# Optimization experiments

Measured on AMD Instinct MI355X. Metric: run time of the kernel, lower is better.

The kernel has to match this reference:

```python
import jax, jax.numpy as jnp
import numpy as np

N = 10000
E = 160000
IN_CH = 128
HID = 128
HEADS = 4
OUT_CH = 1  # forced by nn.Linear(heads, 1) applied after conv2


def _linear_params(key, out_f, in_f):
    k1, k2 = jax.random.split(key)
    bound = 1.0 / np.sqrt(in_f)
    W = jax.random.uniform(k1, (out_f, in_f), jnp.float32, -bound, bound)
    b = jax.random.uniform(k2, (out_f,), jnp.float32, -bound, bound)
    return W, b


def setup_inputs() -> dict:
    key = jax.random.key(0)
    ks = jax.random.split(key, 12)
    x = jax.random.normal(ks[0], (N, IN_CH), jnp.float32)
    edge_index = jax.random.randint(ks[1], (2, E), 0, N, jnp.int64)

    # conv1: TransformerConv(IN_CH, HID, HEADS)
    Wq1, bq1 = _linear_params(ks[2], HEADS * HID, IN_CH)
    Wk1, bk1 = _linear_params(ks[3], HEADS * HID, IN_CH)
    Wv1, bv1 = _linear_params(ks[4], HEADS * HID, IN_CH)
    Ws1, bs1 = _linear_params(ks[5], HEADS * HID, IN_CH)  # root/skip

    # conv2: TransformerConv(HID*HEADS, OUT_CH, HEADS)
    d2 = HID * HEADS
    Wq2, bq2 = _linear_params(ks[6], HEADS * OUT_CH, d2)
    Wk2, bk2 = _linear_params(ks[7], HEADS * OUT_CH, d2)
    Wv2, bv2 = _linear_params(ks[8], HEADS * OUT_CH, d2)
    Ws2, bs2 = _linear_params(ks[9], HEADS * OUT_CH, d2)

    # final nn.Linear(HEADS, 1)
    Wl, bl = _linear_params(ks[10], 1, HEADS)

    return dict(x=x, edge_index=edge_index,
                Wq1=Wq1, bq1=bq1, Wk1=Wk1, bk1=bk1, Wv1=Wv1, bv1=bv1, Ws1=Ws1, bs1=bs1,
                Wq2=Wq2, bq2=bq2, Wk2=Wk2, bk2=bk2, Wv2=Wv2, bv2=bv2, Ws2=Ws2, bs2=bs2,
                Wl=Wl, bl=bl)


def transformer_conv(x, edge_index, Wq, bq, Wk, bk, Wv, bv, Ws, bs, heads, ch):
    # PyG TransformerConv defaults: concat=True, root_weight=True, beta=False
    n = x.shape[0]
    q = (x @ Wq.T + bq).reshape(n, heads, ch)
    k = (x @ Wk.T + bk).reshape(n, heads, ch)
    v = (x @ Wv.T + bv).reshape(n, heads, ch)

    src, dst = edge_index[0], edge_index[1]  # messages flow src -> dst
    # per-edge attention logits [E, H]
    logits = jnp.einsum('ehc,ehc->eh', q[dst], k[src]) / np.sqrt(ch).astype(np.float32)

    # segment softmax over edges grouped by destination node
    seg_max = jax.ops.segment_max(logits, dst, num_segments=n)  # [N, H]
    seg_max = jnp.where(jnp.isfinite(seg_max), seg_max, 0.0)
    ex = jnp.exp(logits - seg_max[dst])
    denom = jax.ops.segment_sum(ex, dst, num_segments=n)  # [N, H]
    alpha = ex / jnp.maximum(denom[dst], 1e-16)  # [E, H]

    # scatter-aggregate weighted values
    msgs = alpha[:, :, None] * v[src]  # [E, H, C]
    out = jax.ops.segment_sum(msgs, dst, num_segments=n)  # [N, H, C]
    out = out.reshape(n, heads * ch)
    # root/skip connection
    return out + (x @ Ws.T + bs)


def reference(x, edge_index,
              Wq1, bq1, Wk1, bk1, Wv1, bv1, Ws1, bs1,
              Wq2, bq2, Wk2, bk2, Wv2, bv2, Ws2, bs2,
              Wl, bl):
    h = transformer_conv(x, edge_index, Wq1, bq1, Wk1, bk1, Wv1, bv1, Ws1, bs1, HEADS, HID)
    h = jax.nn.relu(h)
    # dropout is identity in eval mode
    h = transformer_conv(h, edge_index, Wq2, bq2, Wk2, bk2, Wv2, bv2, Ws2, bs2, HEADS, OUT_CH)
    h = h @ Wl.T + bl  # [N, 1]
    return jnp.mean(h, axis=0, keepdims=True)  # [1, 1]
```

## Files before the change

kernel.cpp:

```cpp
#include <hip/hip_runtime.h>
#include <math.h>

#define NN 10000
#define NE 160000
#define NROWT 79
#define NGEMM (NROWT * 32)

typedef __attribute__((ext_vector_type(8))) short bf16x8;
typedef __attribute__((ext_vector_type(4))) float f32x4;
typedef __attribute__((ext_vector_type(2))) float f32x2;

#if defined(__has_builtin)
#if __has_builtin(__builtin_amdgcn_cvt_pk_fp8_f32) && __has_builtin(__builtin_amdgcn_cvt_pk_f32_fp8)
#define HW_FP8 1
#endif
#endif

__device__ inline ushort f2bf(float x) {
  uint u = __float_as_uint(x);
  return (ushort)((u + 0x7fffu + ((u >> 16) & 1u)) >> 16);
}
__device__ inline uint pk2bf(float a, float b) {
  return (uint)f2bf(a) | ((uint)f2bf(b) << 16);
}

__device__ inline void unpack8(uint4 u, float* f) {
  f[0] = __uint_as_float(u.x << 16); f[1] = __uint_as_float(u.x & 0xffff0000u);
  f[2] = __uint_as_float(u.y << 16); f[3] = __uint_as_float(u.y & 0xffff0000u);
  f[4] = __uint_as_float(u.z << 16); f[5] = __uint_as_float(u.z & 0xffff0000u);
  f[6] = __uint_as_float(u.w << 16); f[7] = __uint_as_float(u.w & 0xffff0000u);
}

#ifndef HW_FP8
__device__ inline float fp8_dec1(uint b) {
  uint s = b >> 7, e = (b >> 3) & 15, m = b & 7;
  float v = (e == 0) ? ldexpf((float)m, -9) : ldexpf((float)(8 + m), (int)e - 10);
  return s ? -v : v;
}
__device__ inline uint fp8_enc1(float x) {
  uint s = (__float_as_uint(x) >> 31) << 7;
  float a = fabsf(x);
  if (!(a < 448.f)) return s | 0x7e;
  if (a < 9.765625e-4f) return s;
  int e; float m = frexpf(a, &e);
  int E = e - 1, q;
  if (E < -6) {
    q = (int)rintf(ldexpf(a, 9));
    if (q == 0) return s;
    if (q >= 8) return s | 8;
    return s | (uint)q;
  }
  q = (int)rintf(ldexpf(m, 4));
  if (q == 16) { q = 8; ++E; }
  if (E > 8 || (E == 8 && q == 15)) return s | 0x7e;
  return s | ((uint)(E + 7) << 3) | (uint)(q - 8);
}
#endif

__device__ inline uint pack4_fp8(float a, float b, float c, float d) {
#ifdef HW_FP8
  uint w = (uint)__builtin_amdgcn_cvt_pk_fp8_f32(a, b, 0, false);
  w = (uint)__builtin_amdgcn_cvt_pk_fp8_f32(c, d, (int)w, true);
  return w;
#else
  return fp8_enc1(a) | (fp8_enc1(b) << 8) | (fp8_enc1(c) << 16) | (fp8_enc1(d) << 24);
#endif
}

__device__ inline void dec8_fp8(uint lo, uint hi, float* f) {
#ifdef HW_FP8
  f32x2 p0 = __builtin_amdgcn_cvt_pk_f32_fp8((int)lo, false);
  f32x2 p1 = __builtin_amdgcn_cvt_pk_f32_fp8((int)lo, true);
  f32x2 p2 = __builtin_amdgcn_cvt_pk_f32_fp8((int)hi, false);
  f32x2 p3 = __builtin_amdgcn_cvt_pk_f32_fp8((int)hi, true);
  f[0] = p0.x; f[1] = p0.y; f[2] = p1.x; f[3] = p1.y;
  f[4] = p2.x; f[5] = p2.y; f[6] = p3.x; f[7] = p3.y;
#else
  f[0] = fp8_dec1(lo & 255); f[1] = fp8_dec1((lo >> 8) & 255);
  f[2] = fp8_dec1((lo >> 16) & 255); f[3] = fp8_dec1(lo >> 24);
  f[4] = fp8_dec1(hi & 255); f[5] = fp8_dec1((hi >> 8) & 255);
  f[6] = fp8_dec1((hi >> 16) & 255); f[7] = fp8_dec1(hi >> 24);
#endif
}

__device__ inline void dec16(uint4 u, float* f) {
  dec8_fp8(u.x, u.y, f);
  dec8_fp8(u.z, u.w, f + 8);
}

__global__ __launch_bounds__(1024) void zero_k(
    int* __restrict__ deg, float* __restrict__ out)
{
  int i = blockIdx.x * 1024 + threadIdx.x;
  if (i < NN) deg[i] = 0;
  if (i == 0) out[0] = 0.f;
}

__global__ __launch_bounds__(256) void prep_k(
    const float* __restrict__ x,
    const float* __restrict__ Wq1, const float* __restrict__ Wk1,
    const float* __restrict__ Wv1, const float* __restrict__ Ws1,
    ushort* __restrict__ x_bf, ushort* __restrict__ w1bf,
    const int* __restrict__ dst, int* __restrict__ deg)
{
  int i = blockIdx.x * 256 + threadIdx.x;
  if (i < NE) atomicAdd(&deg[dst[i]], 1);
  const int n4x = NN * 32;
  const int n4w = 512 * 128 / 4;
  if (i < n4x) {
    float4 v = ((const float4*)x)[i];
    ushort4 o;
    o.x = f2bf(v.x); o.y = f2bf(v.y); o.z = f2bf(v.z); o.w = f2bf(v.w);
    ((ushort4*)x_bf)[i] = o;
  } else {
    int c = i - n4x;
    if (c < 4 * n4w) {
      int seg = c >> 14, k = c & 16383;
      const float* W = (seg == 0) ? Wq1 : (seg == 1) ? Wk1
                     : (seg == 2) ? Wv1 : Ws1;
      float4 v = ((const float4*)W)[k];
      ushort4 o;
      o.x = f2bf(v.x); o.y = f2bf(v.y); o.z = f2bf(v.z); o.w = f2bf(v.w);
      ((ushort4*)(w1bf + ((size_t)seg << 16)))[k] = o;
    }
  }
}

__global__ __launch_bounds__(1024) void scan_k(
    const int* __restrict__ deg, int* __restrict__ rowptr,
    int* __restrict__ cursor)
{
  __shared__ int wsum[16];
  int tid = threadIdx.x;
  int base = tid * 10;
  int loc[10]; int s = 0;
  #pragma unroll
  for (int i = 0; i < 10; ++i) {
    int v = (base + i < NN) ? deg[base + i] : 0;
    loc[i] = s; s += v;
  }
  int mysum = s;
  #pragma unroll
  for (int d = 1; d < 64; d <<= 1) {
    int v = __shfl_up(s, d);
    if ((tid & 63) >= d) s += v;
  }
  if ((tid & 63) == 63) wsum[tid >> 6] = s;
  __syncthreads();
  int woff = 0;
  for (int w = 0; w < (tid >> 6); ++w) woff += wsum[w];
  int excl = woff + s - mysum;
  #pragma unroll
  for (int i = 0; i < 10; ++i) {
    int idx = base + i;
    if (idx < NN) { int r = excl + loc[i]; rowptr[idx] = r; cursor[idx] = r; }
  }
  if (tid == 1023) rowptr[NN] = woff + s;
}

__global__ __launch_bounds__(256) void gemm_scatter(
    const ushort* __restrict__ xbf, const ushort* __restrict__ wbf,
    const float* __restrict__ bq, const float* __restrict__ bk,
    const float* __restrict__ bv, const float* __restrict__ bs,
    unsigned char* __restrict__ q8, unsigned char* __restrict__ kv8,
    ushort* __restrict__ h1b,
    const int* __restrict__ src, const int* __restrict__ dst,
    int* __restrict__ cursor, int* __restrict__ csr_src)
{
  if (blockIdx.x >= NGEMM) {
    int e = (blockIdx.x - NGEMM) * 256 + threadIdx.x;
    if (e < NE) {
      int pos = atomicAdd(&cursor[dst[e]], 1);
      csr_src[pos] = src[e];
    }
    return;
  }
  __shared__ __align__(16) ushort LDSbuf[24576];
  ushort* Al = LDSbuf;
  ushort* Bl = LDSbuf + 16384;
  const int row0 = (blockIdx.x % NROWT) << 7;
  const int ncol0 = (blockIdx.x / NROWT) << 6;
  const int tid = threadIdx.x;

  #pragma unroll
  for (int i = 0; i < 8; ++i) {
    int slot = tid + (i << 8);
    int r = slot >> 4, c = slot & 15;
    int gr = row0 + r;
    uint4 v = make_uint4(0u, 0u, 0u, 0u);
    if (gr < NN) v = *(const uint4*)(xbf + (size_t)gr * 128 + (c << 3));
    *(uint4*)(Al + r * 128 + ((c ^ (r & 7)) << 3)) = v;
  }
  #pragma unroll
  for (int i = 0; i < 4; ++i) {
    int slot = tid + (i << 8);
    int r = slot >> 4, c = slot & 15;
    uint4 v = *(const uint4*)(wbf + (size_t)(ncol0 + r) * 128 + (c << 3));
    *(uint4*)(Bl + r * 128 + ((c ^ (r & 7)) << 3)) = v;
  }
  __syncthreads();

  const int wid = tid >> 6, lane = tid & 63;
  const int wm = wid >> 1, wn = wid & 1;
  const int lr = lane & 15, lkg = lane >> 4;
  const int seg = ncol0 >> 9;
  const int colInSeg = ncol0 & 511;
  const bool swp = (seg < 3);

  f32x4 acc[4][2];
  #pragma unroll
  for (int m = 0; m < 4; ++m)
    #pragma unroll
    for (int n = 0; n < 2; ++n) acc[m][n] = (f32x4){0.f, 0.f, 0.f, 0.f};

  #pragma unroll
  for (int ks = 0; ks < 4; ++ks) {
    int c16 = (ks << 2) + lkg;
    bf16x8 a[4], b[2];
    #pragma unroll
    for (int mf = 0; mf < 4; ++mf) {
      int r = (wm << 6) + (mf << 4) + lr;
      a[mf] = *(const bf16x8*)(Al + r * 128 + ((c16 ^ (r & 7)) << 3));
    }
    #pragma unroll
    for (int nf = 0; nf < 2; ++nf) {
      int r = (wn << 5) + (nf << 4) + lr;
      b[nf] = *(const bf16x8*)(Bl + r * 128 + ((c16 ^ (r & 7)) << 3));
    }
    if (swp) {
      #pragma unroll
      for (int mf = 0; mf < 4; ++mf)
        #pragma unroll
        for (int nf = 0; nf < 2; ++nf)
          acc[mf][nf] = __builtin_amdgcn_mfma_f32_16x16x32_bf16(
              b[nf], a[mf], acc[mf][nf], 0, 0, 0);
    } else {
      #pragma unroll
      for (int mf = 0; mf < 4; ++mf)
        #pragma unroll
        for (int nf = 0; nf < 2; ++nf)
          acc[mf][nf] = __builtin_amdgcn_mfma_f32_16x16x32_bf16(
              a[mf], b[nf], acc[mf][nf], 0, 0, 0);
    }
  }

  __syncthreads();
  float* S = (float*)LDSbuf;
  const float* bias = (seg == 0) ? bq : (seg == 1) ? bk : (seg == 2) ? bv : bs;

  if (swp) {
    const float scale = (seg == 0) ? 0.08838834764831845f : 1.f;
    #pragma unroll
    for (int mf = 0; mf < 4; ++mf) {
      int rl = (wm << 6) + (mf << 4) + lr;
      #pragma unroll
      for (int nf = 0; nf < 2; ++nf) {
        int cl = (wn << 5) + (nf << 4) + (lkg << 2);
        float4 bb = *(const float4*)(bias + colInSeg + cl);
        float4 o;
        o.x = (acc[mf][nf][0] + bb.x) * scale;
        o.y = (acc[mf][nf][1] + bb.y) * scale;
        o.z = (acc[mf][nf][2] + bb.z) * scale;
        o.w = (acc[mf][nf][3] + bb.w) * scale;
        *(float4*)(S + rl * 68 + cl) = o;
      }
    }
    __syncthreads();
    unsigned char* out8 = (seg == 0) ? q8 : kv8;
    const int rs = (seg == 0) ? 512 : 1024;
    const int choff = ((seg == 2) ? 512 : 0) + colInSeg;
    for (int tt = tid; tt < 512; tt += 256) {
      int row = tt >> 2, q4 = (tt & 3) << 4;
      int grow = row0 + row;
      if (grow < NN) {
        const float* p = S + row * 68 + q4;
        uint4 w;
        w.x = pack4_fp8(p[0],  p[1],  p[2],  p[3]);
        w.y = pack4_fp8(p[4],  p[5],  p[6],  p[7]);
        w.z = pack4_fp8(p[8],  p[9],  p[10], p[11]);
        w.w = pack4_fp8(p[12], p[13], p[14], p[15]);
        *(uint4*)(out8 + (size_t)grow * rs + choff + q4) = w;
      }
    }
  } else {
    #pragma unroll
    for (int mf = 0; mf < 4; ++mf) {
      #pragma unroll
      for (int nf = 0; nf < 2; ++nf) {
        int cl = (wn << 5) + (nf << 4) + lr;
        float bb = bias[colInSeg + cl];
        #pragma unroll
        for (int r = 0; r < 4; ++r) {
          int rl = (wm << 6) + (mf << 4) + (lkg << 2) + r;
          S[rl * 68 + cl] = acc[mf][nf][r] + bb;
        }
      }
    }
    __syncthreads();
    {
      int tt = tid;
      int row = tt >> 1, hf = (tt & 1) << 5;
      int grow = row0 + row;
      if (grow < NN) {
        const float* p = S + row * 68 + hf;
        #pragma unroll
        for (int g = 0; g < 4; ++g) {
          uint4 w;
          w.x = pk2bf(p[g*8+0], p[g*8+1]);
          w.y = pk2bf(p[g*8+2], p[g*8+3]);
          w.z = pk2bf(p[g*8+4], p[g*8+5]);
          w.w = pk2bf(p[g*8+6], p[g*8+7]);
          *(uint4*)(h1b + (size_t)grow * 512 + colInSeg + hf + g * 8) = w;
        }
      }
    }
  }
}

#define EDGE_A(kvreg)                                                      \
  {                                                                        \
    float f[16]; dec16(kvreg, f);                                          \
    float t = qf[0]*f[0]+qf[1]*f[1]+qf[2]*f[2]+qf[3]*f[3]                  \
            + qf[4]*f[4]+qf[5]*f[5]+qf[6]*f[6]+qf[7]*f[7]                  \
            + qf[8]*f[8]+qf[9]*f[9]+qf[10]*f[10]+qf[11]*f[11]              \
            + qf[12]*f[12]+qf[13]*f[13]+qf[14]*f[14]+qf[15]*f[15];         \
    t += __shfl_xor(t, 1);                                                 \
    t += __shfl_xor(t, 2);                                                 \
    t += __shfl_xor(t, 4);                                                 \
    float exA = __expf(t);                                                 \
    float exO = __shfl_xor(exA, 32);                                       \
    if (kl) den += exA;                                                    \
    float exV = kl ? 0.f : exO;                                            \
    _Pragma("unroll")                                                      \
    for (int i = 0; i < 16; ++i) acc[i] = fmaf(exV, f[i], acc[i]);         \
  }

__global__ __launch_bounds__(256) void attn1(
    const unsigned char* __restrict__ q8, const unsigned char* __restrict__ kv8,
    const int* __restrict__ rowptr, const int* __restrict__ csr_src,
    ushort* __restrict__ h1b)
{
  const int n = blockIdx.x * 4 + (threadIdx.x >> 6);
  const int lane = threadIdx.x & 63;
  const bool kl = lane < 32;
  const int vl = lane & 31;

  float qf[16];
  if (kl) {
    uint4 qv = *(const uint4*)(q8 + (size_t)n * 512 + (lane << 4));
    dec16(qv, qf);
  } else {
    #pragma unroll
    for (int i = 0; i < 16; ++i) qf[i] = 0.f;
  }

  float acc[16] = {};
  float den = 0.f;
  int j = rowptr[n];
  const int e1 = rowptr[n + 1];
  for (; j + 3 < e1; j += 4) {
    int s0 = csr_src[j], s1 = csr_src[j + 1];
    int s2 = csr_src[j + 2], s3 = csr_src[j + 3];
    uint4 a0 = *(const uint4*)(kv8 + (size_t)s0 * 1024 + (lane << 4));
    uint4 a1 = *(const uint4*)(kv8 + (size_t)s1 * 1024 + (lane << 4));
    uint4 a2 = *(const uint4*)(kv8 + (size_t)s2 * 1024 + (lane << 4));
    uint4 a3 = *(const uint4*)(kv8 + (size_t)s3 * 1024 + (lane << 4));
    EDGE_A(a0)
    EDGE_A(a1)
    EDGE_A(a2)
    EDGE_A(a3)
  }
  for (; j < e1; ++j) {
    int s0 = csr_src[j];
    uint4 a0 = *(const uint4*)(kv8 + (size_t)s0 * 1024 + (lane << 4));
    EDGE_A(a0)
  }

  float dAll = kl ? den : 0.f;
  float dv = __shfl_xor(dAll, 32);
  if (!kl) {
    float inv = 1.f / fmaxf(dv, 1e-16f);
    int c0 = vl << 4;
    float sk[16];
    uint4 s0 = *(const uint4*)(h1b + (size_t)n * 512 + c0);
    uint4 s1 = *(const uint4*)(h1b + (size_t)n * 512 + c0 + 8);
    unpack8(s0, sk); unpack8(s1, sk + 8);
    ushort o[16];
    #pragma unroll
    for (int i = 0; i < 16; ++i)
      o[i] = f2bf(fmaxf(sk[i] + acc[i] * inv, 0.f));
    uint4 w0, w1;
    w0.x = (uint)o[0]  | ((uint)o[1]  << 16);
    w0.y = (uint)o[2]  | ((uint)o[3]  << 16);
    w0.z = (uint)o[4]  | ((uint)o[5]  << 16);
    w0.w = (uint)o[6]  | ((uint)o[7]  << 16);
    w1.x = (uint)o[8]  | ((uint)o[9]  << 16);
    w1.y = (uint)o[10] | ((uint)o[11] << 16);
    w1.z = (uint)o[12] | ((uint)o[13] << 16);
    w1.w = (uint)o[14] | ((uint)o[15] << 16);
    *(uint4*)(h1b + (size_t)n * 512 + c0) = w0;
    *(uint4*)(h1b + (size_t)n * 512 + c0 + 8) = w1;
  }
}

__global__ __launch_bounds__(256) void gemm_l2(
    const ushort* __restrict__ h1b,
    const float* __restrict__ Wq, const float* __restrict__ bq,
    const float* __restrict__ Wk, const float* __restrict__ bk,
    const float* __restrict__ Wv, const float* __restrict__ bv,
    const float* __restrict__ Ws, const float* __restrict__ bs,
    float* __restrict__ qkv2, float* __restrict__ acc2)
{
  __shared__ float red[4][64][17];
  int n0 = blockIdx.x * 64;
  int wid = threadIdx.x >> 6, lane = threadIdx.x & 63;
  int n = n0 + lane;
  const float* Wm[4] = {Wq, Wk, Wv, Ws};
  float s[16] = {};
  if (n < NN) {
    const ushort* a = h1b + (size_t)n * 512 + wid * 128;
    #pragma unroll 2
    for (int i = 0; i < 128; i += 8) {
      uint4 hv = *(const uint4*)(a + i);
      float av[8]; unpack8(hv, av);
      #pragma unroll
      for (int j = 0; j < 16; ++j) {
        const float* w = Wm[j >> 2] + (size_t)(j & 3) * 512 + wid * 128 + i;
        s[j] += av[0]*w[0] + av[1]*w[1] + av[2]*w[2] + av[3]*w[3]
              + av[4]*w[4] + av[5]*w[5] + av[6]*w[6] + av[7]*w[7];
      }
    }
  }
  #pragma unroll
  for (int j = 0; j < 16; ++j) red[wid][lane][j] = s[j];
  __syncthreads();
  #pragma unroll
  for (int q = 0; q < 4; ++q) {
    int idx = threadIdx.x * 4 + q;
    int ln = idx >> 4, j = idx & 15;
    int nn2 = n0 + ln;
    if (nn2 >= NN) continue;
    float v = red[0][ln][j] + red[1][ln][j] + red[2][ln][j] + red[3][ln][j];
    int sg = j >> 2, r = j & 3;
    const float* bb = (sg == 0) ? bq : (sg == 1) ? bk : (sg == 2) ? bv : bs;
    v += bb[r];
    if (sg < 3) qkv2[nn2 * 12 + sg * 4 + r] = v;
    else        acc2[nn2 * 4 + r] = v;
  }
}

__global__ __launch_bounds__(256) void attn2_final(
    const float* __restrict__ qkv2, const int* __restrict__ rowptr,
    const int* __restrict__ csr_src, const float* __restrict__ acc2,
    const float* __restrict__ Wl, const float* __restrict__ bl,
    float* __restrict__ out)
{
  __shared__ float red[4];
  int t = blockIdx.x * 256 + threadIdx.x;
  int n = t >> 4, h = (t >> 2) & 3, part = t & 3;
  float q = qkv2[n * 12 + h];
  float den = 0.f, acc = 0.f;
  int e1 = rowptr[n + 1];
  for (int j = rowptr[n] + part; j < e1; j += 4) {
    int s = csr_src[j];
    float k = qkv2[s * 12 + 4 + h];
    float v = qkv2[s * 12 + 8 + h];
    float ex = __expf(q * k);
    den += ex; acc += ex * v;
  }
  den += __shfl_xor(den, 1); acc += __shfl_xor(acc, 1);
  den += __shfl_xor(den, 2); acc += __shfl_xor(acc, 2);
  float c = 0.f;
  if (part == 0)
    c = (acc2[n * 4 + h] + acc / fmaxf(den, 1e-16f)) * Wl[h] * (1.0f / NN);
  if (t == 0) c += bl[0];
  c += __shfl_xor(c, 4);
  c += __shfl_xor(c, 8);
  c += __shfl_xor(c, 16);
  c += __shfl_xor(c, 32);
  if ((threadIdx.x & 63) == 0) red[threadIdx.x >> 6] = c;
  __syncthreads();
  if (threadIdx.x == 0)
    unsafeAtomicAdd(out, red[0] + red[1] + red[2] + red[3]);
}

extern "C" void kernel_launch(void* const* d_in, const int* in_sizes, int n_in,
                              void* d_out, int out_size, void* d_ws, size_t ws_size,
                              hipStream_t stream)
{
  const float* x   = (const float*)d_in[0];
  const int*   ei  = (const int*)d_in[1];
  const float *Wq1 = (const float*)d_in[2],  *bq1 = (const float*)d_in[3];
  const float *Wk1 = (const float*)d_in[4],  *bk1 = (const float*)d_in[5];
  const float *Wv1 = (const float*)d_in[6],  *bv1 = (const float*)d_in[7];
  const float *Ws1 = (const float*)d_in[8],  *bs1 = (const float*)d_in[9];
  const float *Wq2 = (const float*)d_in[10], *bq2 = (const float*)d_in[11];
  const float *Wk2 = (const float*)d_in[12], *bk2 = (const float*)d_in[13];
  const float *Wv2 = (const float*)d_in[14], *bv2 = (const float*)d_in[15];
  const float *Ws2 = (const float*)d_in[16], *bs2 = (const float*)d_in[17];
  const float *Wl  = (const float*)d_in[18], *bl  = (const float*)d_in[19];
  const int* srcp = ei;
  const int* dstp = ei + NE;

  unsigned char* q8  = (unsigned char*)d_ws;
  unsigned char* kv8 = q8 + (size_t)NN * 512;
  ushort* x_bf = (ushort*)(kv8 + (size_t)NN * 1024);
  ushort* w1bf = x_bf + (size_t)NN * 128;
  ushort* h1b  = w1bf + (size_t)2048 * 128;
  float*  qkv2 = (float*)(h1b + (size_t)NN * 512);
  float*  acc2 = qkv2 + (size_t)NN * 12;
  int*   deg     = (int*)(acc2 + (size_t)NN * 4);
  int*   rowptr  = deg + NN;
  int*   cursor  = rowptr + NN + 1;
  int*   csr_src = cursor + NN;

  zero_k<<<10, 1024, 0, stream>>>(deg, (float*)d_out);
  {
    const int total = NN * 32 + 4 * (512 * 128 / 4);
    prep_k<<<(total + 255) / 256, 256, 0, stream>>>(
        x, Wq1, Wk1, Wv1, Ws1, x_bf, w1bf, dstp, deg);
  }
  scan_k<<<1, 1024, 0, stream>>>(deg, rowptr, cursor);

  gemm_scatter<<<NGEMM + (NE + 255) / 256, 256, 0, stream>>>(
      x_bf, w1bf, bq1, bk1, bv1, bs1, q8, kv8, h1b,
      srcp, dstp, cursor, csr_src);

  attn1<<<NN / 4, 256, 0, stream>>>(q8, kv8, rowptr, csr_src, h1b);

  gemm_l2<<<(NN + 63) / 64, 256, 0, stream>>>(
      h1b, Wq2, bq2, Wk2, bk2, Wv2, bv2, Ws2, bs2, qkv2, acc2);

  attn2_final<<<NN * 16 / 256, 256, 0, stream>>>(
      qkv2, rowptr, csr_src, acc2, Wl, bl, (float*)d_out);
}
```

Before: 131.6 us.

## Widen GEMM column tile to 128 and unroll edge gather loop by eight

The GEMM tile grows from 128x64 to 128x128 output columns, halving the number of GEMM blocks. Each wave now computes 32 rows by 128 columns, so every A fragment is reused across more B fragments, and the epilogue drains through LDS in two passes. The attention edge loop is unrolled to eight outstanding KV gathers per iteration to expose more memory-level parallelism. In exchange the kernel uses more LDS and more accumulator registers, which may lower occupancy, and the two-pass epilogue adds extra barriers.

After: 131.2 us, median of 3. About the same (-0.3%).

```diff
diff --git a/kernel.cpp b/kernel.cpp
--- a/kernel.cpp
+++ b/kernel.cpp
@@ -4,7 +4,8 @@
 #define NN 10000
 #define NE 160000
 #define NROWT 79
-#define NGEMM (NROWT * 32)
+#define NCOLT 16
+#define NGEMM (NROWT * NCOLT)
 
 typedef __attribute__((ext_vector_type(8))) short bf16x8;
 typedef __attribute__((ext_vector_type(4))) float f32x4;
@@ -175,11 +176,11 @@
     }
     return;
   }
-  __shared__ __align__(16) ushort LDSbuf[24576];
+  __shared__ __align__(16) ushort LDSbuf[32768];
   ushort* Al = LDSbuf;
   ushort* Bl = LDSbuf + 16384;
   const int row0 = (blockIdx.x % NROWT) << 7;
-  const int ncol0 = (blockIdx.x / NROWT) << 6;
+  const int ncol0 = (blockIdx.x / NROWT) << 7;
   const int tid = threadIdx.x;
 
   #pragma unroll
@@ -192,7 +193,7 @@
     *(uint4*)(Al + r * 128 + ((c ^ (r & 7)) << 3)) = v;
   }
   #pragma unroll
-  for (int i = 0; i < 4; ++i) {
+  for (int i = 0; i < 8; ++i) {
     int slot = tid + (i << 8);
     int r = slot >> 4, c = slot & 15;
     uint4 v = *(const uint4*)(wbf + (size_t)(ncol0 + r) * 128 + (c << 3));
@@ -200,45 +201,44 @@
   }
   __syncthreads();
 
-  const int wid = tid >> 6, lane = tid & 63;
-  const int wm = wid >> 1, wn = wid & 1;
+  const int wv = tid >> 6, lane = tid & 63;
   const int lr = lane & 15, lkg = lane >> 4;
   const int seg = ncol0 >> 9;
   const int colInSeg = ncol0 & 511;
   const bool swp = (seg < 3);
 
-  f32x4 acc[4][2];
-  #pragma unroll
-  for (int m = 0; m < 4; ++m)
-    #pragma unroll
-    for (int n = 0; n < 2; ++n) acc[m][n] = (f32x4){0.f, 0.f, 0.f, 0.f};
+  f32x4 acc[2][8];
+  #pragma unroll
+  for (int m = 0; m < 2; ++m)
+    #pragma unroll
+    for (int n = 0; n < 8; ++n) acc[m][n] = (f32x4){0.f, 0.f, 0.f, 0.f};
 
   #pragma unroll
   for (int ks = 0; ks < 4; ++ks) {
     int c16 = (ks << 2) + lkg;
-    bf16x8 a[4], b[2];
-    #pragma unroll
-    for (int mf = 0; mf < 4; ++mf) {
-      int r = (wm << 6) + (mf << 4) + lr;
+    bf16x8 a[2], b[8];
+    #pragma unroll
+    for (int mf = 0; mf < 2; ++mf) {
+      int r = (wv << 5) + (mf << 4) + lr;
       a[mf] = *(const bf16x8*)(Al + r * 128 + ((c16 ^ (r & 7)) << 3));
     }
     #pragma unroll
-    for (int nf = 0; nf < 2; ++nf) {
-      int r = (wn << 5) + (nf << 4) + lr;
+    for (int nf = 0; nf < 8; ++nf) {
+      int r = (nf << 4) + lr;
       b[nf] = *(const bf16x8*)(Bl + r * 128 + ((c16 ^ (r & 7)) << 3));
     }
     if (swp) {
       #pragma unroll
-      for (int mf = 0; mf < 4; ++mf)
+      for (int mf = 0; mf < 2; ++mf)
         #pragma unroll
-        for (int nf = 0; nf < 2; ++nf)
+        for (int nf = 0; nf < 8; ++nf)
           acc[mf][nf] = __builtin_amdgcn_mfma_f32_16x16x32_bf16(
               b[nf], a[mf], acc[mf][nf], 0, 0, 0);
     } else {
       #pragma unroll
-      for (int mf = 0; mf < 4; ++mf)
+      for (int mf = 0; mf < 2; ++mf)
         #pragma unroll
-        for (int nf = 0; nf < 2; ++nf)
+        for (int nf = 0; nf < 8; ++nf)
           acc[mf][nf] = __builtin_amdgcn_mfma_f32_16x16x32_bf16(
               a[mf], b[nf], acc[mf][nf], 0, 0, 0);
     }
@@ -250,69 +250,75 @@
 
   if (swp) {
     const float scale = (seg == 0) ? 0.08838834764831845f : 1.f;
-    #pragma unroll
-    for (int mf = 0; mf < 4; ++mf) {
-      int rl = (wm << 6) + (mf << 4) + lr;
-      #pragma unroll
-      for (int nf = 0; nf < 2; ++nf) {
-        int cl = (wn << 5) + (nf << 4) + (lkg << 2);
-        float4 bb = *(const float4*)(bias + colInSeg + cl);
-        float4 o;
-        o.x = (acc[mf][nf][0] + bb.x) * scale;
-        o.y = (acc[mf][nf][1] + bb.y) * scale;
-        o.z = (acc[mf][nf][2] + bb.z) * scale;
-        o.w = (acc[mf][nf][3] + bb.w) * scale;
-        *(float4*)(S + rl * 68 + cl) = o;
-      }
-    }
-    __syncthreads();
     unsigned char* out8 = (seg == 0) ? q8 : kv8;
     const int rs = (seg == 0) ? 512 : 1024;
     const int choff = ((seg == 2) ? 512 : 0) + colInSeg;
-    for (int tt = tid; tt < 512; tt += 256) {
-      int row = tt >> 2, q4 = (tt & 3) << 4;
-      int grow = row0 + row;
-      if (grow < NN) {
-        const float* p = S + row * 68 + q4;
-        uint4 w;
-        w.x = pack4_fp8(p[0],  p[1],  p[2],  p[3]);
-        w.y = pack4_fp8(p[4],  p[5],  p[6],  p[7]);
-        w.z = pack4_fp8(p[8],  p[9],  p[10], p[11]);
-        w.w = pack4_fp8(p[12], p[13], p[14], p[15]);
-        *(uint4*)(out8 + (size_t)grow * rs + choff + q4) = w;
-      }
-    }
-  } else {
-    #pragma unroll
-    for (int mf = 0; mf < 4; ++mf) {
+    #pragma unroll
+    for (int pass = 0; pass < 2; ++pass) {
       #pragma unroll
-      for (int nf = 0; nf < 2; ++nf) {
-        int cl = (wn << 5) + (nf << 4) + lr;
-        float bb = bias[colInSeg + cl];
+      for (int mf = 0; mf < 2; ++mf) {
+        int rl = (wv << 5) + (mf << 4) + lr;
         #pragma unroll
-        for (int r = 0; r < 4; ++r) {
-          int rl = (wm << 6) + (mf << 4) + (lkg << 2) + r;
-          S[rl * 68 + cl] = acc[mf][nf][r] + bb;
+        for (int nf2 = 0; nf2 < 4; ++nf2) {
+          int nf = (pass << 2) + nf2;
+          int cl = (nf << 4) + (lkg << 2);
+          float4 bb = *(const float4*)(bias + colInSeg + cl);
+          float4 o;
+          o.x = (acc[mf][nf][0] + bb.x) * scale;
+          o.y = (acc[mf][nf][1] + bb.y) * scale;
+          o.z = (acc[mf][nf][2] + bb.z) * scale;
+          o.w = (acc[mf][nf][3] + bb.w) * scale;
+          *(float4*)(S + rl * 68 + (cl - (pass << 6))) = o;
         }
       }
-    }
-    __syncthreads();
-    {
-      int tt = tid;
-      int row = tt >> 1, hf = (tt & 1) << 5;
-      int grow = row0 + row;
-      if (grow < NN) {
-        const float* p = S + row * 68 + hf;
-        #pragma unroll
-        for (int g = 0; g < 4; ++g) {
+      __syncthreads();
+      for (int tt = tid; tt < 512; tt += 256) {
+        int row = tt >> 2, q4 = (tt & 3) << 4;
+        int grow = row0 + row;
+        if (grow < NN) {
+          const float* p = S + row * 68 + q4;
           uint4 w;
-          w.x = pk2bf(p[g*8+0], p[g*8+1]);
-          w.y = pk2bf(p[g*8+2], p[g*8+3]);
-          w.z = pk2bf(p[g*8+4], p[g*8+5]);
-          w.w = pk2bf(p[g*8+6], p[g*8+7]);
-          *(uint4*)(h1b + (size_t)grow * 512 + colInSeg + hf + g * 8) = w;
+          w.x = pack4_fp8(p[0],  p[1],  p[2],  p[3]);
+          w.y = pack4_fp8(p[4],  p[5],  p[6],  p[7]);
+          w.z = pack4_fp8(p[8],  p[9],  p[10], p[11]);
+          w.w = pack4_fp8(p[12], p[13], p[14], p[15]);
+          *(uint4*)(out8 + (size_t)grow * rs + choff + (pass << 6) + q4) = w;
         }
       }
+      __syncthreads();
+    }
+  } else {
+    #pragma unroll
+    for (int pass = 0; pass < 2; ++pass) {
+      #pragma unroll
+      for (int mf = 0; mf < 2; ++mf) {
+        #pragma unroll
+        for (int nf2 = 0; nf2 < 4; ++nf2) {
+          int nf = (pass << 2) + nf2;
+          int cl = (nf << 4) + lr;
+          float bb = bias[colInSeg + cl];
+          #pragma unroll
+          for (int r = 0; r < 4; ++r) {
+            int rl = (wv << 5) + (mf << 4) + (lkg << 2) + r;
+            S[rl * 68 + (cl - (pass << 6))] = acc[mf][nf][r] + bb;
+          }
+        }
+      }
+      __syncthreads();
+      for (int tt = tid; tt < 1024; tt += 256) {
+        int row = tt >> 3, g = tt & 7;
+        int grow = row0 + row;
+        if (grow < NN) {
+          const float* p = S + row * 68 + (g << 3);
+          uint4 w;
+          w.x = pk2bf(p[0], p[1]);
+          w.y = pk2bf(p[2], p[3]);
+          w.z = pk2bf(p[4], p[5]);
+          w.w = pk2bf(p[6], p[7]);
+          *(uint4*)(h1b + (size_t)grow * 512 + colInSeg + (pass << 6) + (g << 3)) = w;
+        }
+      }
+      __syncthreads();
     }
   }
 }
@@ -358,21 +364,36 @@
   float den = 0.f;
   int j = rowptr[n];
   const int e1 = rowptr[n + 1];
-  for (; j + 3 < e1; j += 4) {
-    int s0 = csr_src[j], s1 = csr_src[j + 1];
-    int s2 = csr_src[j + 2], s3 = csr_src[j + 3];
-    uint4 a0 = *(const uint4*)(kv8 + (size_t)s0 * 1024 + (lane << 4));
-    uint4 a1 = *(const uint4*)(kv8 + (size_t)s1 * 1024 + (lane << 4));
-    uint4 a2 = *(const uint4*)(kv8 + (size_t)s2 * 1024 + (lane << 4));
-    uint4 a3 = *(const uint4*)(kv8 + (size_t)s3 * 1024 + (lane << 4));
+  for (; j + 7 < e1; j += 8) {
+    uint4 a0 = *(const uint4*)(kv8 + (size_t)csr_src[j + 0] * 1024 + (lane << 4));
+    uint4 a1 = *(const uint4*)(kv8 + (size_t)csr_src[j + 1] * 1024 + (lane << 4));
+    uint4 a2 = *(const uint4*)(kv8 + (size_t)csr_src[j + 2] * 1024 + (lane << 4));
+    uint4 a3 = *(const uint4*)(kv8 + (size_t)csr_src[j + 3] * 1024 + (lane << 4));
+    uint4 a4 = *(const uint4*)(kv8 + (size_t)csr_src[j + 4] * 1024 + (lane << 4));
+    uint4 a5 = *(const uint4*)(kv8 + (size_t)csr_src[j + 5] * 1024 + (lane << 4));
+    uint4 a6 = *(const uint4*)(kv8 + (size_t)csr_src[j + 6] * 1024 + (lane << 4));
+    uint4 a7 = *(const uint4*)(kv8 + (size_t)csr_src[j + 7] * 1024 + (lane << 4));
     EDGE_A(a0)
     EDGE_A(a1)
     EDGE_A(a2)
     EDGE_A(a3)
+    EDGE_A(a4)
+    EDGE_A(a5)
+    EDGE_A(a6)
+    EDGE_A(a7)
+  }
+  for (; j + 3 < e1; j += 4) {
+    uint4 a0 = *(const uint4*)(kv8 + (size_t)csr_src[j + 0] * 1024 + (lane << 4));
+    uint4 a1 = *(const uint4*)(kv8 + (size_t)csr_src[j + 1] * 1024 + (lane << 4));
+    uint4 a2 = *(const uint4*)(kv8 + (size_t)csr_src[j + 2] * 1024 + (lane << 4));
+    uint4 a3 = *(const uint4*)(kv8 + (size_t)csr_src[j + 3] * 1024 + (lane << 4));
+    EDGE_A(a0)
+    EDGE_A(a1)
+    EDGE_A(a2)
+    EDGE_A(a3)
   }
   for (; j < e1; ++j) {
-    int s0 = csr_src[j];
-    uint4 a0 = *(const uint4*)(kv8 + (size_t)s0 * 1024 + (lane << 4));
+    uint4 a0 = *(const uint4*)(kv8 + (size_t)csr_src[j] * 1024 + (lane << 4));
     EDGE_A(a0)
   }
 
```
